# Kernel tuning notes

Measured on AMD Instinct MI355X. Metric: run time of the kernel, lower is better.

Reference implementation:

```python
import jax, jax.numpy as jnp
import numpy as np

N_NODES = 100000
N_EDGES = 1600000
HID = 128


def setup_inputs() -> dict:
    key = jax.random.key(0)
    k1, k2, k3, k4, k5 = jax.random.split(key, 5)
    node_embeddings = jax.random.normal(k1, (N_NODES, HID), dtype=jnp.float32)
    src_idx = jax.random.randint(k2, (N_EDGES,), 0, N_NODES, dtype=jnp.int64)
    tgt_idx = jax.random.randint(k3, (N_EDGES,), 0, N_NODES, dtype=jnp.int64)
    # Params of the selected edge-type predictor (Linear(2h,h) -> ReLU -> Linear(h,1))
    W1 = jax.random.normal(k4, (2 * HID, HID), dtype=jnp.float32) * (1.0 / np.sqrt(2 * HID))
    b1 = jnp.zeros((HID,), dtype=jnp.float32)
    W2 = jax.random.normal(k5, (HID, 1), dtype=jnp.float32) * (1.0 / np.sqrt(HID))
    b2 = jnp.zeros((1,), dtype=jnp.float32)
    return {
        "node_embeddings": node_embeddings,
        "src_idx": src_idx,
        "tgt_idx": tgt_idx,
        "edge_type_idx": 0,
        "W1": W1,
        "b1": b1,
        "W2": W2,
        "b2": b2,
    }


def reference(node_embeddings, src_idx, tgt_idx, edge_type_idx, W1, b1, W2, b2):
    # edge_type_idx selects a predictor; params passed in are that predictor's.
    src_emb = node_embeddings[src_idx]  # [E, H]
    tgt_emb = node_embeddings[tgt_idx]  # [E, H]
    # cat([src,tgt]) @ W1 == src @ W1[:H] + tgt @ W1[H:]  (avoids materializing pair_feat)
    h = jax.nn.relu(src_emb @ W1[:HID] + tgt_emb @ W1[HID:] + b1)  # [E, H]
    out = h @ W2 + b2  # [E, 1]
    return out[:, 0]  # squeeze(-1) -> [E]
```

## Files before the change

### kernel.cpp

```cpp
#include <hip/hip_runtime.h>
#include <hip/hip_bf16.h>

#define HID 128

typedef __attribute__((ext_vector_type(8))) short short8;
typedef __attribute__((ext_vector_type(4))) float f32x4;
typedef __attribute__((ext_vector_type(16))) float f32x16;
typedef __attribute__((ext_vector_type(4))) unsigned int u32x4;
typedef __attribute__((ext_vector_type(2))) _Float16 h2;

__device__ __forceinline__ short f2bf(float x) {
    __bf16 b = (__bf16)x;
    return __builtin_bit_cast(short, b);
}


__global__ void pack_w1_uv_kernel(const float* __restrict__ W1, short* __restrict__ bpk2) {
    int t = blockIdx.x * 256 + threadIdx.x;
    int l    = t & 63;
    int ks   = (t >> 6) & 7;
    int nt   = (t >> 9) & 3;
    int half = t >> 11;
    int k0  = half * 128 + ks * 16 + (l >> 5) * 8;
    int col = nt * 32 + (l & 31);
    short8 v;
#pragma unroll
    for (int j = 0; j < 8; ++j)
        v[j] = f2bf(W1[(k0 + j) * HID + col]);
    *reinterpret_cast<short8*>(&bpk2[t * 8]) = v;
}

__global__ __launch_bounds__(512, 4) void uv_kernel(
    const float* __restrict__ emb,
    const short* __restrict__ bpk2,
    unsigned short* __restrict__ U,
    unsigned short* __restrict__ V,
    int Nn)
{
    __shared__ short lds_b[32768];

    const int tid = threadIdx.x;
    const int l   = tid & 63;
    const int wid = tid >> 6;
    const int wg  = wid >> 1;
    const int wn  = wid & 1;
    const int lc  = l & 31;
    const int hi  = l >> 5;

    {
        const u32x4* g = (const u32x4*)bpk2;
        u32x4* d = (u32x4*)lds_b;
#pragma unroll
        for (int i = 0; i < 8; ++i) d[i * 512 + tid] = g[i * 512 + tid];
    }
    __syncthreads();

    const int base = blockIdx.x * 128 + wg * 32;
    int nr = base + lc;
    if (nr >= Nn) nr = Nn - 1;

    f32x16 accU[2], accV[2];
#pragma unroll
    for (int n = 0; n < 2; ++n) { accU[n] = (f32x16)(0.f); accV[n] = (f32x16)(0.f); }

#pragma unroll
    for (int ks = 0; ks < 8; ++ks) {
        const float* p = emb + (size_t)nr * HID + ks * 16 + hi * 8;
        f32x4 x0 = *reinterpret_cast<const f32x4*>(p);
        f32x4 x1 = *reinterpret_cast<const f32x4*>(p + 4);
        short8 afr;
#pragma unroll
        for (int j = 0; j < 4; ++j) { afr[j] = f2bf(x0[j]); afr[4 + j] = f2bf(x1[j]); }
#pragma unroll
        for (int n = 0; n < 2; ++n) {
            const int nt = wn * 2 + n;
            short8 bU = *reinterpret_cast<const short8*>(&lds_b[(((0 + nt) * 8 + ks) * 64 + l) * 8]);
            short8 bV = *reinterpret_cast<const short8*>(&lds_b[(((4 + nt) * 8 + ks) * 64 + l) * 8]);
            accU[n] = __builtin_amdgcn_mfma_f32_32x32x16_bf16(afr, bU, accU[n], 0, 0, 0);
            accV[n] = __builtin_amdgcn_mfma_f32_32x32x16_bf16(afr, bV, accV[n], 0, 0, 0);
        }
    }

#pragma unroll
    for (int n = 0; n < 2; ++n) {
        const int col = wn * 64 + n * 32 + lc;
#pragma unroll
        for (int r = 0; r < 16; ++r) {
            const int row = (r & 3) + 8 * (r >> 2) + 4 * hi;
            const int node = base + row;
            if (node < Nn) {
                _Float16 hu = (_Float16)accU[n][r];
                _Float16 hv = (_Float16)accV[n][r];
                U[(size_t)node * HID + col] = __builtin_bit_cast(unsigned short, hu);
                V[(size_t)node * HID + col] = __builtin_bit_cast(unsigned short, hv);
            }
        }
    }
}

__global__ __launch_bounds__(256) void hist64_kernel(
    const void* __restrict__ src_raw, const void* __restrict__ tgt_raw,
    int E, float bscale, int* __restrict__ gh)
{
    __shared__ int lh[64];
    const int tid = threadIdx.x;
    if (tid < 64) lh[tid] = 0;
    __syncthreads();

    int i64f = 1;
    {
        const int* s32 = (const int*)src_raw;
#pragma unroll
        for (int i = 1; i < 32; i += 2) i64f &= (s32[i] == 0);
    }
    const int stride = gridDim.x * 256;
    for (int e = blockIdx.x * 256 + tid; e < E; e += stride) {
        int t = i64f ? (int)((const long long*)tgt_raw)[e]
                     : ((const int*)tgt_raw)[e];
        int b = (int)((float)t * bscale);
        b = b < 0 ? 0 : (b > 63 ? 63 : b);
        atomicAdd(&lh[b], 1);
    }
    __syncthreads();
    if (tid < 64 && lh[tid]) atomicAdd(&gh[tid], lh[tid]);
}

__global__ void off64_kernel(const int* __restrict__ gh,
                             int* __restrict__ goff, int* __restrict__ off8) {
    __shared__ int h[64];
    const int t = threadIdx.x;
    h[t] = gh[t];
    __syncthreads();
    if (t == 0) {
        int acc = 0;
        for (int b = 0; b < 64; ++b) {
            goff[b] = acc;
            if ((b & 7) == 0) off8[b >> 3] = acc;
            acc += h[b];
        }
        off8[8] = acc;
    }
}

__global__ __launch_bounds__(256) void scatter64_kernel(
    const void* __restrict__ src_raw, const void* __restrict__ tgt_raw,
    int E, float bscale,
    const int* __restrict__ goff, int* __restrict__ cursor,
    int* __restrict__ ss, int* __restrict__ tt, int* __restrict__ ei)
{
    __shared__ int lh[64], lh2[64], lo[64], grb[64], go[64];
    __shared__ int sS[2048], sT[2048], sE[2048], bk[2048];

    const int tid = threadIdx.x;
    int i64f = 1;
    {
        const int* s32 = (const int*)src_raw;
#pragma unroll
        for (int i = 1; i < 32; i += 2) i64f &= (s32[i] == 0);
    }
    if (tid < 64) { lh[tid] = 0; lh2[tid] = 0; go[tid] = goff[tid]; }
    __syncthreads();

    const int base = blockIdx.x * 2048;
    int myS[8], myT[8], myB[8];
#pragma unroll
    for (int k = 0; k < 8; ++k) {
        const int e = base + k * 256 + tid;
        myB[k] = -1;
        if (e < E) {
            int s, t;
            if (i64f) {
                s = (int)((const long long*)src_raw)[e];
                t = (int)((const long long*)tgt_raw)[e];
            } else {
                s = ((const int*)src_raw)[e];
                t = ((const int*)tgt_raw)[e];
            }
            int b = (int)((float)t * bscale);
            b = b < 0 ? 0 : (b > 63 ? 63 : b);
            myS[k] = s; myT[k] = t; myB[k] = b;
            atomicAdd(&lh[b], 1);
        }
    }
    __syncthreads();
    if (tid == 0) {
        int acc = 0;
        for (int b = 0; b < 64; ++b) { lo[b] = acc; acc += lh[b]; }
    }
    __syncthreads();
    if (tid < 64 && lh[tid] > 0) grb[tid] = atomicAdd(&cursor[tid], lh[tid]);
    __syncthreads();
#pragma unroll
    for (int k = 0; k < 8; ++k) {
        if (myB[k] >= 0) {
            const int b = myB[k];
            const int pl = lo[b] + atomicAdd(&lh2[b], 1);
            sS[pl] = myS[k];
            sT[pl] = myT[k];
            sE[pl] = base + k * 256 + tid;
            bk[pl] = b;
        }
    }
    __syncthreads();
    const int total = lo[63] + lh[63];
    for (int i = tid; i < total; i += 256) {
        const int b = bk[i];
        const int dst = go[b] + grb[b] + (i - lo[b]);
        ss[dst] = sS[i];
        tt[dst] = sT[i];
        ei[dst] = sE[i];
    }
}

__global__ __launch_bounds__(256) void edge_pass_part_kernel(
    const unsigned short* __restrict__ U,
    const unsigned short* __restrict__ V,
    const int* __restrict__ ss,
    const int* __restrict__ tt,
    const int* __restrict__ ei,
    const int* __restrict__ off8,
    const float* __restrict__ b1,
    const float* __restrict__ W2,
    const float* __restrict__ b2,
    float* __restrict__ out,
    int per_x)
{
    const int tid = threadIdx.x;
    const int l   = tid & 63;
    const int wid = tid >> 6;
    const int le  = l >> 4;
    const int lc  = l & 15;
    const int p   = blockIdx.x & 7;
    const int r   = blockIdx.x >> 3;

    const int pbeg = off8[p];
    const int pend = off8[p + 1];

    h2 b1p[4], w2p[4];
    {
        f32x4 a = *reinterpret_cast<const f32x4*>(b1 + lc * 8);
        f32x4 b = *reinterpret_cast<const f32x4*>(b1 + lc * 8 + 4);
        f32x4 c = *reinterpret_cast<const f32x4*>(W2 + lc * 8);
        f32x4 d = *reinterpret_cast<const f32x4*>(W2 + lc * 8 + 4);
#pragma unroll
        for (int j = 0; j < 2; ++j) {
            b1p[0][j] = (_Float16)a[j];     b1p[1][j] = (_Float16)a[2 + j];
            b1p[2][j] = (_Float16)b[j];     b1p[3][j] = (_Float16)b[2 + j];
            w2p[0][j] = (_Float16)c[j];     w2p[1][j] = (_Float16)c[2 + j];
            w2p[2][j] = (_Float16)d[j];     w2p[3][j] = (_Float16)d[2 + j];
        }
    }
    const float b2s = b2[0];
    const h2 zero2 = (h2)((_Float16)0.f);

    for (int base = pbeg + r * 64; base < pend; base += per_x * 64) {
        short8 ub[4], vb[4];
        int oid[4];
        bool live[4];
#pragma unroll
        for (int g = 0; g < 4; ++g) {
            int pos = base + wid * 16 + g * 4 + le;
            live[g] = (pos < pend);
            if (!live[g]) pos = base;
            const int s = ss[pos];
            const int t = tt[pos];
            oid[g] = ei[pos];
            ub[g] = *reinterpret_cast<const short8*>(U + (unsigned)s * HID + lc * 8);
            vb[g] = *reinterpret_cast<const short8*>(V + (unsigned)t * HID + lc * 8);
        }

#pragma unroll
        for (int g = 0; g < 4; ++g) {
            const unsigned int* uw = (const unsigned int*)&ub[g];
            const unsigned int* vw = (const unsigned int*)&vb[g];
            h2 s2 = zero2;
#pragma unroll
            for (int j = 0; j < 4; ++j) {
                h2 hu = __builtin_bit_cast(h2, uw[j]);
                h2 hv = __builtin_bit_cast(h2, vw[j]);
                h2 h  = hu + hv + b1p[j];
                h = __builtin_elementwise_max(h, zero2);
                s2 = s2 + h * w2p[j];
            }
            float s = (float)s2[0] + (float)s2[1];
#pragma unroll
            for (int w = 1; w < 16; w <<= 1)
                s += __shfl_xor(s, w, 16);
            if (lc == 0 && live[g])
                out[oid[g]] = s + b2s;
        }
    }
}

__global__ __launch_bounds__(256) void edge_pass_kernel(
    const unsigned short* __restrict__ U,
    const unsigned short* __restrict__ V,
    const void* __restrict__ src_raw,
    const void* __restrict__ tgt_raw,
    const float* __restrict__ b1,
    const float* __restrict__ W2,
    const float* __restrict__ b2,
    float* __restrict__ out,
    int E)
{
    const int tid = threadIdx.x;
    const int l   = tid & 63;
    const int wid = tid >> 6;
    const int le  = l >> 4;
    const int lc  = l & 15;

    int oddw = 0;
    {
        const int* s32 = (const int*)src_raw;
        if (l < 32) oddw = s32[2 * l + 1];
    }
    const bool i64f = (__ballot(oddw != 0) == 0ULL);

    h2 b1p[4], w2p[4];
    {
        f32x4 a = *reinterpret_cast<const f32x4*>(b1 + lc * 8);
        f32x4 b = *reinterpret_cast<const f32x4*>(b1 + lc * 8 + 4);
        f32x4 c = *reinterpret_cast<const f32x4*>(W2 + lc * 8);
        f32x4 d = *reinterpret_cast<const f32x4*>(W2 + lc * 8 + 4);
#pragma unroll
        for (int j = 0; j < 2; ++j) {
            b1p[0][j] = (_Float16)a[j];     b1p[1][j] = (_Float16)a[2 + j];
            b1p[2][j] = (_Float16)b[j];     b1p[3][j] = (_Float16)b[2 + j];
            w2p[0][j] = (_Float16)c[j];     w2p[1][j] = (_Float16)c[2 + j];
            w2p[2][j] = (_Float16)d[j];     w2p[3][j] = (_Float16)d[2 + j];
        }
    }
    const float b2s = b2[0];
    const h2 zero2 = (h2)((_Float16)0.f);

    const long long ebase = ((long long)blockIdx.x * 4 + wid) * 16;

    short8 ub[4], vb[4];
#pragma unroll
    for (int g = 0; g < 4; ++g) {
        long long e = ebase + g * 4 + le;
        if (e >= E) e = E - 1;
        long long si, ti;
        if (i64f) {
            si = ((const long long*)src_raw)[e];
            ti = ((const long long*)tgt_raw)[e];
        } else {
            si = ((const int*)src_raw)[e];
            ti = ((const int*)tgt_raw)[e];
        }
        ub[g] = *reinterpret_cast<const short8*>(U + (unsigned)si * HID + lc * 8);
        vb[g] = *reinterpret_cast<const short8*>(V + (unsigned)ti * HID + lc * 8);
    }

#pragma unroll
    for (int g = 0; g < 4; ++g) {
        const unsigned int* uw = (const unsigned int*)&ub[g];
        const unsigned int* vw = (const unsigned int*)&vb[g];
        h2 s2 = zero2;
#pragma unroll
        for (int j = 0; j < 4; ++j) {
            h2 hu = __builtin_bit_cast(h2, uw[j]);
            h2 hv = __builtin_bit_cast(h2, vw[j]);
            h2 h  = hu + hv + b1p[j];
            h = __builtin_elementwise_max(h, zero2);
            s2 = s2 + h * w2p[j];
        }
        float s = (float)s2[0] + (float)s2[1];
#pragma unroll
        for (int w = 1; w < 16; w <<= 1)
            s += __shfl_xor(s, w, 16);
        const long long e = ebase + g * 4 + le;
        if (lc == 0 && e < E)
            out[e] = s + b2s;
    }
}


__global__ void pack_w1_kernel(const float* __restrict__ W1, short* __restrict__ bpk) {
    int t = blockIdx.x * 256 + threadIdx.x;
    int f = (t >> 6) & 7;
    int l = t & 63;
    int n = t >> 9;
    int c = l & 15, kb = l >> 4;
    int k0 = f * 32 + kb * 8;
    short8 v;
#pragma unroll
    for (int j = 0; j < 8; ++j)
        v[j] = f2bf(W1[(k0 + j) * HID + n * 16 + c]);
    *reinterpret_cast<short8*>(&bpk[t * 8]) = v;
}

__global__ __launch_bounds__(256) void conv_emb_kernel(
    const float* __restrict__ emb, short* __restrict__ bemb, int n8) {
    int i = blockIdx.x * 256 + threadIdx.x;
    if (i >= n8) return;
    f32x4 x0 = *reinterpret_cast<const f32x4*>(emb + (size_t)i * 8);
    f32x4 x1 = *reinterpret_cast<const f32x4*>(emb + (size_t)i * 8 + 4);
    short8 v;
#pragma unroll
    for (int j = 0; j < 4; ++j) {
        v[j]     = f2bf(x0[j]);
        v[4 + j] = f2bf(x1[j]);
    }
    *reinterpret_cast<short8*>(&bemb[(size_t)i * 8]) = v;
}

template <int MODE>
__global__ __launch_bounds__(512, 4) void edge_head_kernel(
    const float* __restrict__ emb,
    const short* __restrict__ bemb,
    const void* __restrict__ src_raw,
    const void* __restrict__ tgt_raw,
    const float* __restrict__ W1,
    const float* __restrict__ b1,
    const float* __restrict__ W2,
    const float* __restrict__ b2,
    const short* __restrict__ bpk,
    float* __restrict__ out,
    int E)
{
    __shared__ short lds_b[32768];

    const int tid = threadIdx.x;

    int i64f = 1;
    {
        const int* s32 = (const int*)src_raw;
#pragma unroll
        for (int i = 1; i < 32; i += 2) i64f &= (s32[i] == 0);
    }

    if (MODE != 2) {
        const u32x4* g = (const u32x4*)bpk;
        u32x4* d = (u32x4*)lds_b;
#pragma unroll
        for (int i = 0; i < 8; ++i) d[i * 512 + tid] = g[i * 512 + tid];
    } else {
        for (int i = 0; i < 64; ++i) {
            int idx = i * 512 + tid;
            int col = idx & 127;
            int k   = idx >> 7;
            int n = col >> 4, cc = col & 15;
            int f = k >> 5, kb = (k >> 3) & 3, j = k & 7;
            int l2 = kb * 16 + cc;
            lds_b[(((n * 8 + f) * 64 + l2) << 3) + j] = f2bf(W1[idx]);
        }
    }
    __syncthreads();

    const int l = tid & 63;
    const int wid = tid >> 6;
    const int c = l & 15;
    const int g = l >> 4;
    const long long e0 = (long long)blockIdx.x * 256 + wid * 32;

    unsigned so[2], to[2];
#pragma unroll
    for (int m = 0; m < 2; ++m) {
        long long e = e0 + m * 16 + c;
        if (e >= E) e = E - 1;
        long long si, ti;
        if (i64f) {
            si = ((const long long*)src_raw)[e];
            ti = ((const long long*)tgt_raw)[e];
        } else {
            si = ((const int*)src_raw)[e];
            ti = ((const int*)tgt_raw)[e];
        }
        so[m] = (unsigned)si * HID;
        to[m] = (unsigned)ti * HID;
    }

    f32x4 acc[2][8];
#pragma unroll
    for (int m = 0; m < 2; ++m)
#pragma unroll
        for (int n = 0; n < 8; ++n)
            acc[m][n] = (f32x4){0.f, 0.f, 0.f, 0.f};

    const int koff = g * 8;
#pragma unroll
    for (int f = 0; f < 8; ++f) {
        short8 afr[2];
        const int k0 = (f & 3) * 32 + koff;
#pragma unroll
        for (int m = 0; m < 2; ++m) {
            const unsigned off = (f < 4 ? so[m] : to[m]) + k0;
            if (MODE == 0) {
                afr[m] = *reinterpret_cast<const short8*>(bemb + off);
            } else {
                f32x4 x0 = *reinterpret_cast<const f32x4*>(emb + off);
                f32x4 x1 = *reinterpret_cast<const f32x4*>(emb + off + 4);
                short8 t;
#pragma unroll
                for (int j = 0; j < 4; ++j) {
                    t[j]     = f2bf(x0[j]);
                    t[4 + j] = f2bf(x1[j]);
                }
                afr[m] = t;
            }
        }
#pragma unroll
        for (int n = 0; n < 8; ++n) {
            short8 bfr = *reinterpret_cast<const short8*>(&lds_b[((n * 8 + f) * 64 + l) * 8]);
#pragma unroll
            for (int m = 0; m < 2; ++m)
                acc[m][n] = __builtin_amdgcn_mfma_f32_16x16x32_bf16(afr[m], bfr, acc[m][n], 0, 0, 0);
        }
    }

    float b1v[8], w2v[8];
#pragma unroll
    for (int n = 0; n < 8; ++n) {
        b1v[n] = b1[n * 16 + c];
        w2v[n] = W2[n * 16 + c];
    }
    const float b2s = b2[0];

#pragma unroll
    for (int m = 0; m < 2; ++m) {
        float s[4] = {0.f, 0.f, 0.f, 0.f};
#pragma unroll
        for (int n = 0; n < 8; ++n) {
#pragma unroll
            for (int r = 0; r < 4; ++r)
                s[r] += fmaxf(acc[m][n][r] + b1v[n], 0.f) * w2v[n];
        }
#pragma unroll
        for (int w = 1; w < 16; w <<= 1) {
#pragma unroll
            for (int r = 0; r < 4; ++r)
                s[r] += __shfl_xor(s[r], w, 16);
        }
        if (c == 0) {
            const long long eb = e0 + m * 16 + g * 4;
#pragma unroll
            for (int r = 0; r < 4; ++r)
                if (eb + r < E) out[eb + r] = s[r] + b2s;
        }
    }
}

extern "C" void kernel_launch(void* const* d_in, const int* in_sizes, int n_in,
                              void* d_out, int out_size, void* d_ws, size_t ws_size,
                              hipStream_t stream) {
    const float* emb = (const float*)d_in[0];
    const void*  src = d_in[1];
    const void*  tgt = d_in[2];
    const float* W1 = (const float*)d_in[4];
    const float* b1 = (const float*)d_in[5];
    const float* W2 = (const float*)d_in[6];
    const float* b2 = (const float*)d_in[7];
    float* out = (float*)d_out;

    const int E  = in_sizes[1];
    const int Nn = in_sizes[0] / HID;

    const size_t uv_bytes = (size_t)Nn * HID * sizeof(short);
    const size_t off_gh   = 65536;
    const size_t off_cur  = off_gh + 256;
    const size_t off_goff = off_cur + 256;
    const size_t off_off8 = off_goff + 256;
    const size_t off_U    = 65536 + 4096;
    const size_t off_V    = off_U + uv_bytes;
    const size_t off_ss   = off_V + uv_bytes;
    const size_t off_tt   = off_ss + (size_t)E * 4;
    const size_t off_ei   = off_tt + (size_t)E * 4;
    const size_t need_part = off_ei + (size_t)E * 4;
    const size_t need_uv   = 65536 + 2 * uv_bytes;
    const size_t need_old  = 65536 + (size_t)in_sizes[0] * sizeof(short);

    if (ws_size >= need_part && E >= 4096) {
        short*          bpk2   = (short*)d_ws;
        int*            gh     = (int*)((char*)d_ws + off_gh);
        int*            cursor = (int*)((char*)d_ws + off_cur);
        int*            goff   = (int*)((char*)d_ws + off_goff);
        int*            off8   = (int*)((char*)d_ws + off_off8);
        unsigned short* U      = (unsigned short*)((char*)d_ws + off_U);
        unsigned short* Vv     = (unsigned short*)((char*)d_ws + off_V);
        int*            ss     = (int*)((char*)d_ws + off_ss);
        int*            tt     = (int*)((char*)d_ws + off_tt);
        int*            ei     = (int*)((char*)d_ws + off_ei);

        const float bscale = 63.9999f / (float)Nn;

        hipMemsetAsync((char*)d_ws + off_gh, 0, 512, stream);
        pack_w1_uv_kernel<<<16, 256, 0, stream>>>(W1, bpk2);
        hist64_kernel<<<256, 256, 0, stream>>>(src, tgt, E, bscale, gh);
        uv_kernel<<<(Nn + 127) / 128, 512, 0, stream>>>(emb, bpk2, U, Vv, Nn);
        off64_kernel<<<1, 64, 0, stream>>>(gh, goff, off8);
        scatter64_kernel<<<(E + 2047) / 2048, 256, 0, stream>>>(
            src, tgt, E, bscale, goff, cursor, ss, tt, ei);
        const int per_x = (E / 8 + 4096) / 64 + 2;
        edge_pass_part_kernel<<<per_x * 8, 256, 0, stream>>>(
            U, Vv, ss, tt, ei, off8, b1, W2, b2, out, per_x);
        return;
    }

    if (ws_size >= need_uv) {
        short*          bpk2 = (short*)d_ws;
        unsigned short* U    = (unsigned short*)((char*)d_ws + 65536);
        unsigned short* Vv   = (unsigned short*)((char*)d_ws + 65536 + uv_bytes);

        pack_w1_uv_kernel<<<16, 256, 0, stream>>>(W1, bpk2);
        uv_kernel<<<(Nn + 127) / 128, 512, 0, stream>>>(emb, bpk2, U, Vv, Nn);
        edge_pass_kernel<<<(E + 63) / 64, 256, 0, stream>>>(U, Vv, src, tgt, b1, W2, b2, out, E);
        return;
    }

    short* bpk  = (short*)d_ws;
    short* bemb = (short*)((char*)d_ws + 65536);

    int mode;
    if (ws_size >= need_old)        mode = 0;
    else if (ws_size >= 65536)      mode = 1;
    else                            mode = 2;

    if (mode != 2)
        pack_w1_kernel<<<16, 256, 0, stream>>>(W1, bpk);
    if (mode == 0) {
        const int n8 = in_sizes[0] / 8;
        conv_emb_kernel<<<(n8 + 255) / 256, 256, 0, stream>>>(emb, bemb, n8);
    }

    const int grid = (E + 255) / 256;
    if (mode == 0)
        edge_head_kernel<0><<<grid, 512, 0, stream>>>(emb, bemb, src, tgt, W1, b1, W2, b2, bpk, out, E);
    else if (mode == 1)
        edge_head_kernel<1><<<grid, 512, 0, stream>>>(emb, bemb, src, tgt, W1, b1, W2, b2, bpk, out, E);
    else
        edge_head_kernel<2><<<grid, 512, 0, stream>>>(emb, bemb, src, tgt, W1, b1, W2, b2, bpk, out, E);
}
```

Measured before the change: 150.2 us.

## Drop memset and offset kernel, fuse prefix sums, pack src/tgt pairs

Removes the hipMemsetAsync and the single-block off64 kernel. Zeroing moves into pack_w1_uv_kernel, and the 64-bin prefix sums are computed with wave shuffles inside scatter and edge_pass. Source and target indices are stored as one int2 array, so the edge pass issues one 8-byte load per edge instead of two, and shared staging uses a byte bucket array. This cuts launch and serialization overhead, at the cost of every edge block redundantly scanning the histogram.

```diff
diff --git a/kernel.cpp b/kernel.cpp
--- a/kernel.cpp
+++ b/kernel.cpp
@@ -15,7 +15,9 @@
 }
 
 
-__global__ void pack_w1_uv_kernel(const float* __restrict__ W1, short* __restrict__ bpk2) {
+__global__ void pack_w1_uv_kernel(const float* __restrict__ W1, short* __restrict__ bpk2,
+                                  int* __restrict__ zero128) {
+    if (zero128 && blockIdx.x == 0 && threadIdx.x < 128) zero128[threadIdx.x] = 0;
     int t = blockIdx.x * 256 + threadIdx.x;
     int l    = t & 63;
     int ks   = (t >> 6) & 7;
@@ -125,31 +127,16 @@
     if (tid < 64 && lh[tid]) atomicAdd(&gh[tid], lh[tid]);
 }
 
-__global__ void off64_kernel(const int* __restrict__ gh,
-                             int* __restrict__ goff, int* __restrict__ off8) {
-    __shared__ int h[64];
-    const int t = threadIdx.x;
-    h[t] = gh[t];
-    __syncthreads();
-    if (t == 0) {
-        int acc = 0;
-        for (int b = 0; b < 64; ++b) {
-            goff[b] = acc;
-            if ((b & 7) == 0) off8[b >> 3] = acc;
-            acc += h[b];
-        }
-        off8[8] = acc;
-    }
-}
-
 __global__ __launch_bounds__(256) void scatter64_kernel(
     const void* __restrict__ src_raw, const void* __restrict__ tgt_raw,
     int E, float bscale,
-    const int* __restrict__ goff, int* __restrict__ cursor,
-    int* __restrict__ ss, int* __restrict__ tt, int* __restrict__ ei)
+    const int* __restrict__ gh, int* __restrict__ cursor,
+    int2* __restrict__ st, int* __restrict__ ei)
 {
     __shared__ int lh[64], lh2[64], lo[64], grb[64], go[64];
-    __shared__ int sS[2048], sT[2048], sE[2048], bk[2048];
+    __shared__ int2 sST[2048];
+    __shared__ int sE[2048];
+    __shared__ unsigned char bkk[2048];
 
     const int tid = threadIdx.x;
     int i64f = 1;
@@ -158,7 +145,7 @@
 #pragma unroll
         for (int i = 1; i < 32; i += 2) i64f &= (s32[i] == 0);
     }
-    if (tid < 64) { lh[tid] = 0; lh2[tid] = 0; go[tid] = goff[tid]; }
+    if (tid < 64) { lh[tid] = 0; lh2[tid] = 0; }
     __syncthreads();
 
     const int base = blockIdx.x * 2048;
@@ -183,31 +170,36 @@
         }
     }
     __syncthreads();
-    if (tid == 0) {
-        int acc = 0;
-        for (int b = 0; b < 64; ++b) { lo[b] = acc; acc += lh[b]; }
-    }
-    __syncthreads();
-    if (tid < 64 && lh[tid] > 0) grb[tid] = atomicAdd(&cursor[tid], lh[tid]);
+    if (tid < 64) {
+        int vl = lh[tid], vg = gh[tid];
+        int il = vl, ig = vg;
+#pragma unroll
+        for (int off = 1; off < 64; off <<= 1) {
+            int xl = __shfl_up(il, off, 64);
+            int xg = __shfl_up(ig, off, 64);
+            if (tid >= off) { il += xl; ig += xg; }
+        }
+        lo[tid] = il - vl;
+        go[tid] = ig - vg;
+        grb[tid] = (vl > 0) ? atomicAdd(&cursor[tid], vl) : 0;
+    }
     __syncthreads();
 #pragma unroll
     for (int k = 0; k < 8; ++k) {
         if (myB[k] >= 0) {
             const int b = myB[k];
             const int pl = lo[b] + atomicAdd(&lh2[b], 1);
-            sS[pl] = myS[k];
-            sT[pl] = myT[k];
+            sST[pl] = make_int2(myS[k], myT[k]);
             sE[pl] = base + k * 256 + tid;
-            bk[pl] = b;
+            bkk[pl] = (unsigned char)b;
         }
     }
     __syncthreads();
     const int total = lo[63] + lh[63];
     for (int i = tid; i < total; i += 256) {
-        const int b = bk[i];
+        const int b = bkk[i];
         const int dst = go[b] + grb[b] + (i - lo[b]);
-        ss[dst] = sS[i];
-        tt[dst] = sT[i];
+        st[dst] = sST[i];
         ei[dst] = sE[i];
     }
 }
@@ -215,17 +207,31 @@
 __global__ __launch_bounds__(256) void edge_pass_part_kernel(
     const unsigned short* __restrict__ U,
     const unsigned short* __restrict__ V,
-    const int* __restrict__ ss,
-    const int* __restrict__ tt,
+    const int2* __restrict__ st,
     const int* __restrict__ ei,
-    const int* __restrict__ off8,
+    const int* __restrict__ gh,
     const float* __restrict__ b1,
     const float* __restrict__ W2,
     const float* __restrict__ b2,
     float* __restrict__ out,
     int per_x)
 {
+    __shared__ int sh_off8[9];
+
     const int tid = threadIdx.x;
+    if (tid < 64) {
+        int v = gh[tid];
+        int inc = v;
+#pragma unroll
+        for (int off = 1; off < 64; off <<= 1) {
+            int x = __shfl_up(inc, off, 64);
+            if (tid >= off) inc += x;
+        }
+        if ((tid & 7) == 0) sh_off8[tid >> 3] = inc - v;
+        if (tid == 63) sh_off8[8] = inc;
+    }
+    __syncthreads();
+
     const int l   = tid & 63;
     const int wid = tid >> 6;
     const int le  = l >> 4;
@@ -233,8 +239,8 @@
     const int p   = blockIdx.x & 7;
     const int r   = blockIdx.x >> 3;
 
-    const int pbeg = off8[p];
-    const int pend = off8[p + 1];
+    const int pbeg = sh_off8[p];
+    const int pend = sh_off8[p + 1];
 
     h2 b1p[4], w2p[4];
     {
@@ -262,11 +268,10 @@
             int pos = base + wid * 16 + g * 4 + le;
             live[g] = (pos < pend);
             if (!live[g]) pos = base;
-            const int s = ss[pos];
-            const int t = tt[pos];
+            const int2 pr = st[pos];
             oid[g] = ei[pos];
-            ub[g] = *reinterpret_cast<const short8*>(U + (unsigned)s * HID + lc * 8);
-            vb[g] = *reinterpret_cast<const short8*>(V + (unsigned)t * HID + lc * 8);
+            ub[g] = *reinterpret_cast<const short8*>(U + (unsigned)pr.x * HID + lc * 8);
+            vb[g] = *reinterpret_cast<const short8*>(V + (unsigned)pr.y * HID + lc * 8);
         }
 
 #pragma unroll
@@ -558,14 +563,10 @@
 
     const size_t uv_bytes = (size_t)Nn * HID * sizeof(short);
     const size_t off_gh   = 65536;
-    const size_t off_cur  = off_gh + 256;
-    const size_t off_goff = off_cur + 256;
-    const size_t off_off8 = off_goff + 256;
     const size_t off_U    = 65536 + 4096;
     const size_t off_V    = off_U + uv_bytes;
-    const size_t off_ss   = off_V + uv_bytes;
-    const size_t off_tt   = off_ss + (size_t)E * 4;
-    const size_t off_ei   = off_tt + (size_t)E * 4;
+    const size_t off_st   = off_V + uv_bytes;
+    const size_t off_ei   = off_st + (size_t)E * 8;
     const size_t need_part = off_ei + (size_t)E * 4;
     const size_t need_uv   = 65536 + 2 * uv_bytes;
     const size_t need_old  = 65536 + (size_t)in_sizes[0] * sizeof(short);
@@ -573,27 +574,22 @@
     if (ws_size >= need_part && E >= 4096) {
         short*          bpk2   = (short*)d_ws;
         int*            gh     = (int*)((char*)d_ws + off_gh);
-        int*            cursor = (int*)((char*)d_ws + off_cur);
-        int*            goff   = (int*)((char*)d_ws + off_goff);
-        int*            off8   = (int*)((char*)d_ws + off_off8);
+        int*            cursor = gh + 64;
         unsigned short* U      = (unsigned short*)((char*)d_ws + off_U);
         unsigned short* Vv     = (unsigned short*)((char*)d_ws + off_V);
-        int*            ss     = (int*)((char*)d_ws + off_ss);
-        int*            tt     = (int*)((char*)d_ws + off_tt);
+        int2*           st     = (int2*)((char*)d_ws + off_st);
         int*            ei     = (int*)((char*)d_ws + off_ei);
 
         const float bscale = 63.9999f / (float)Nn;
 
-        hipMemsetAsync((char*)d_ws + off_gh, 0, 512, stream);
-        pack_w1_uv_kernel<<<16, 256, 0, stream>>>(W1, bpk2);
+        pack_w1_uv_kernel<<<16, 256, 0, stream>>>(W1, bpk2, gh);
         hist64_kernel<<<256, 256, 0, stream>>>(src, tgt, E, bscale, gh);
         uv_kernel<<<(Nn + 127) / 128, 512, 0, stream>>>(emb, bpk2, U, Vv, Nn);
-        off64_kernel<<<1, 64, 0, stream>>>(gh, goff, off8);
         scatter64_kernel<<<(E + 2047) / 2048, 256, 0, stream>>>(
-            src, tgt, E, bscale, goff, cursor, ss, tt, ei);
+            src, tgt, E, bscale, gh, cursor, st, ei);
         const int per_x = (E / 8 + 4096) / 64 + 2;
         edge_pass_part_kernel<<<per_x * 8, 256, 0, stream>>>(
-            U, Vv, ss, tt, ei, off8, b1, W2, b2, out, per_x);
+            U, Vv, st, ei, gh, b1, W2, b2, out, per_x);
         return;
     }
 
@@ -602,7 +598,7 @@
         unsigned short* U    = (unsigned short*)((char*)d_ws + 65536);
         unsigned short* Vv   = (unsigned short*)((char*)d_ws + 65536 + uv_bytes);
 
-        pack_w1_uv_kernel<<<16, 256, 0, stream>>>(W1, bpk2);
+        pack_w1_uv_kernel<<<16, 256, 0, stream>>>(W1, bpk2, nullptr);
         uv_kernel<<<(Nn + 127) / 128, 512, 0, stream>>>(emb, bpk2, U, Vv, Nn);
         edge_pass_kernel<<<(E + 63) / 64, 256, 0, stream>>>(U, Vv, src, tgt, b1, W2, b2, out, E);
         return;
```

New measurement: 147.5 us. No clear change (-1.8%).
